# Kernel tuning notes

Measured on AMD Instinct MI355X. Metric: run time of the kernel, lower is better.

Reference implementation:

```python
import jax, jax.numpy as jnp
import numpy as np

NUM_NODES = 100000
NUM_EDGES = 100000
NNZ = 1600000
D_IN = 64
D_OUT = 64


def setup_inputs() -> dict:
    key = jax.random.key(0)
    k1, k2, k3, k4 = jax.random.split(key, 4)
    X = jax.random.normal(k1, (NUM_NODES, D_IN), dtype=jnp.float32)
    V = jax.random.randint(k2, (NNZ,), 0, NUM_NODES, dtype=jnp.int64)
    E = jax.random.randint(k3, (NNZ,), 0, NUM_EDGES, dtype=jnp.int64)
    S_features = jnp.zeros((1,), dtype=jnp.float32)  # unused by forward
    W = jax.random.normal(k4, (D_OUT, D_IN), dtype=jnp.float32) / np.sqrt(D_IN)
    b = jnp.zeros((D_OUT,), dtype=jnp.float32)
    return {"X": X, "V": V, "E": E, "S_features": S_features, "W": W, "b": b}


def reference(X, V, E, S_features, W, b):
    # linear projection (nn.Linear stores W as [out, in])
    Xp = X @ W.T + b                                   # [N, D_out]

    ones = jnp.ones((V.shape[0],), dtype=jnp.float32)
    cnt_e = jax.ops.segment_sum(ones, E, num_segments=NUM_EDGES)   # edge sizes
    D_v = jax.ops.segment_sum(ones, V, num_segments=NUM_NODES)     # node degrees

    # Y = scatter_mean(X[V], E): per-hyperedge mean of member node features
    Xve = Xp[V]                                        # [nnz, D_out]
    Y = jax.ops.segment_sum(Xve, E, num_segments=NUM_EDGES)
    Y = Y / jnp.maximum(cnt_e, 1.0)[:, None]

    # _De: torch scatter_reduce(reduce='mean', include_self=True) over zeros:
    # mean includes the initial self value 0 -> sum / (count + 1)
    De_sum = jax.ops.segment_sum(D_v[V], E, num_segments=NUM_EDGES)
    De = De_sum / (cnt_e + 1.0)
    De_inv = jnp.where(De > 0, jax.lax.rsqrt(jnp.maximum(De, 1e-30)), 1.0)
    Y = De_inv[:, None] * Y

    # scatter back to nodes
    Xev = Y[E]                                         # [nnz, D_out]
    Xn = jax.ops.segment_sum(Xev, V, num_segments=NUM_NODES)
    Dv_inv = jnp.where(D_v > 0, jax.lax.rsqrt(jnp.maximum(D_v, 1e-30)), 0.0)
    out = Dv_inv[:, None] * Xn                         # [N, D_out]
    # is_last=True: no relu / dropout
    return out
```

## Files before the change

### kernel.cpp

```cpp
#include <hip/hip_runtime.h>
#include <hip/hip_bf16.h>

#define NUM_NODES 100000
#define NUM_EDGES 100000
#define NNZ       1600000
#define D         64

#define BKT     128
#define NBKT_E  ((NUM_EDGES + BKT - 1) / BKT)
#define NBKT_V  ((NUM_NODES + BKT - 1) / BKT)
#define NBKT_TOT (NBKT_E + NBKT_V)
#define CAP     2816

#define TILE 8192
#define NT_SIDE ((NNZ + TILE - 1) / TILE)

#define GEMM_ROWS 32
#define NGEMM (NUM_NODES / GEMM_ROWS)

__device__ inline unsigned pack_bf16x2(float a, float b) {
  unsigned ua = __float_as_uint(a), ub = __float_as_uint(b);
  ua = (ua + 0x7fffu + ((ua >> 16) & 1u)) >> 16;
  ub = (ub + 0x7fffu + ((ub >> 16) & 1u)) >> 16;
  return ua | (ub << 16);
}
__device__ inline void unpack_acc(unsigned u, float& lo, float& hi) {
  lo = __uint_as_float(u << 16);
  hi = __uint_as_float(u & 0xffff0000u);
}
__device__ inline void acc_row(const uint4& w, float* acc) {
  float lo, hi;
  unpack_acc(w.x, lo, hi); acc[0] += lo; acc[1] += hi;
  unpack_acc(w.y, lo, hi); acc[2] += lo; acc[3] += hi;
  unpack_acc(w.z, lo, hi); acc[4] += lo; acc[5] += hi;
  unpack_acc(w.w, lo, hi); acc[6] += lo; acc[7] += hi;
}

__global__ __launch_bounds__(1024, 4) void bin_tile_k(
    const int* __restrict__ V, const int* __restrict__ E,
    int* __restrict__ curb, unsigned* __restrict__ pair) {
  __shared__ unsigned stage[TILE];
  __shared__ unsigned short stageb[TILE];
  __shared__ int hist[NBKT_E];
  __shared__ int gbase[NBKT_E];
  __shared__ int lcur[NBKT_E];
  __shared__ int wsum[16];

  const int t = threadIdx.x;
  const int side = (blockIdx.x >= NT_SIDE) ? 1 : 0;
  const int bt = blockIdx.x - side * NT_SIDE;
  const int j0 = bt * TILE;
  const int n = (NNZ - j0 < TILE) ? (NNZ - j0) : TILE;
  const int cbase = side ? NBKT_E : 0;

  for (int i = t; i < NBKT_E; i += 1024) hist[i] = 0;
  __syncthreads();

  int vj[8], ej[8];
#pragma unroll
  for (int k = 0; k < 8; ++k) {
    const int jj = t + k * 1024;
    int v = -1, e = 0;
    if (jj < n) {
      v = V[j0 + jj];
      e = E[j0 + jj];
    }
    vj[k] = v; ej[k] = e;
    if (v >= 0) atomicAdd(&hist[(side ? v : e) >> 7], 1);
  }
  __syncthreads();

  {
    const int lane = t & 63, wid = t >> 6;
    const int cb = (t < NBKT_E) ? hist[t] : 0;
    int s = cb;
#pragma unroll
    for (int d = 1; d < 64; d <<= 1) {
      const int y = __shfl_up(s, d, 64);
      if (lane >= d) s += y;
    }
    if (lane == 63) wsum[wid] = s;
    __syncthreads();
    if (wid == 0) {
      int ws = (lane < 16) ? wsum[lane] : 0;
#pragma unroll
      for (int d = 1; d < 16; d <<= 1) {
        const int y = __shfl_up(ws, d, 64);
        if (lane >= d) ws += y;
      }
      if (lane < 16) wsum[lane] = ws;
    }
    __syncthreads();
    const int incl = s + (wid > 0 ? wsum[wid - 1] : 0);
    if (t < NBKT_E) {
      const int excl = incl - cb;
      lcur[t] = excl;
      const int rb = cb ? atomicAdd(&curb[cbase + t], cb) : 0;
      gbase[t] = (cbase + t) * CAP + rb - excl;
    }
  }
  __syncthreads();

#pragma unroll
  for (int k = 0; k < 8; ++k) {
    const int v = vj[k];
    if (v >= 0) {
      const int e = ej[k];
      const int key = side ? v : e;
      const int src = side ? e : v;
      const int b = key >> 7;
      const unsigned w = ((unsigned)src << 7) | (unsigned)(key & 127);
      const int pos = atomicAdd(&lcur[b], 1);
      stage[pos] = w;
      stageb[pos] = (unsigned short)b;
    }
  }
  __syncthreads();

  for (int sI = t; sI < n; sI += 1024) {
    pair[gbase[stageb[sI]] + sI] = stage[sI];
  }
}

#define DG_SMEM 24832
__global__ __launch_bounds__(256) void deg_gemm_k(
    const int* __restrict__ curb, const unsigned* __restrict__ pair,
    int* __restrict__ cnt_v,
    const float* __restrict__ X, const float* __restrict__ W,
    const float* __restrict__ bvec, unsigned short* __restrict__ Xpb) {
  __shared__ __align__(16) char smem[DG_SMEM];
  const int t = threadIdx.x;

  if (blockIdx.x < NBKT_V) {
    int* rcnt = (int*)smem;
    const int b = blockIdx.x;
    const int base = (NBKT_E + b) * CAP;
    int n = curb[NBKT_E + b];
    if (n > CAP) n = CAP;
    if (t < BKT) rcnt[t] = 0;
    __syncthreads();
    for (int j = t; j < n; j += 256) {
      atomicAdd(&rcnt[pair[base + j] & 127u], 1);
    }
    __syncthreads();
    const int v = b * BKT + t;
    if (t < BKT && v < NUM_NODES) cnt_v[v] = rcnt[t];
  } else {
    float* Wl = (float*)smem;
    float* Xl = (float*)(smem + 16640);
    const int g = blockIdx.x - NBKT_V;

    for (int j = t; j < D * D; j += 256) Wl[(j >> 6) * 65 + (j & 63)] = W[j];
    const int row0 = g * GEMM_ROWS;
    const float4* X4 = (const float4*)(X + (size_t)row0 * D);
    float4* Xl4 = (float4*)Xl;
    for (int j = t; j < GEMM_ROWS * (D / 4); j += 256) Xl4[j] = X4[j];
    __syncthreads();

    const int c = t & 63;
    const int rq = t >> 6;
    float acc[8];
#pragma unroll
    for (int i = 0; i < 8; ++i) acc[i] = 0.f;
#pragma unroll
    for (int k = 0; k < D; ++k) {
      const float w = Wl[c * 65 + k];
#pragma unroll
      for (int i = 0; i < 8; ++i)
        acc[i] = fmaf(Xl[(rq + i * 4) * D + k], w, acc[i]);
    }
    const float bias = bvec[c];
#pragma unroll
    for (int i = 0; i < 8; ++i) {
      const int r = row0 + rq + i * 4;
      const float v = acc[i] + bias;
      unsigned u = __float_as_uint(v);
      u = (u + 0x7fffu + ((u >> 16) & 1u)) >> 16;
      Xpb[(size_t)r * D + c] = (unsigned short)u;
    }
  }
}

__global__ __launch_bounds__(512) void edge_fused_k(
    const int* __restrict__ curb, const unsigned* __restrict__ pair,
    const int* __restrict__ cnt_v, const uint4* __restrict__ Xpb,
    uint4* __restrict__ Yb) {
  __shared__ unsigned seg[CAP];
  __shared__ int sorted_[CAP];
  __shared__ int rcnt[BKT];
  __shared__ int sc[BKT];
  __shared__ int lcur[BKT];
  const int b = blockIdx.x, t = threadIdx.x;
  const int base = b * CAP;
  int n = curb[b];
  if (n > CAP) n = CAP;
  const int e0 = b * BKT;
  const int nrows = (NUM_EDGES - e0 < BKT) ? (NUM_EDGES - e0) : BKT;

  if (t < BKT) rcnt[t] = 0;
  __syncthreads();

  for (int j = t; j < n; j += 512) {
    const unsigned w = pair[base + j];
    seg[j] = w;
    atomicAdd(&rcnt[w & 127u], 1);
  }
  __syncthreads();

  if (t < 64) {
    const int a = rcnt[2 * t], bb = rcnt[2 * t + 1];
    int s = a + bb;
#pragma unroll
    for (int d = 1; d < 64; d <<= 1) {
      const int y = __shfl_up(s, d, 64);
      if (t >= d) s += y;
    }
    sc[2 * t + 1] = s;
    sc[2 * t] = s - bb;
    lcur[2 * t + 1] = s - bb;
    lcur[2 * t] = s - bb - a;
  }
  __syncthreads();

  for (int j = t; j < n; j += 512) {
    const unsigned w = seg[j];
    const int pos = atomicAdd(&lcur[w & 127u], 1);
    sorted_[pos] = (int)(w >> 7);
  }
  __syncthreads();

  const int q = t & 7;
#pragma unroll
  for (int rr = 0; rr < 2; ++rr) {
    const int row = (t >> 3) + rr * 64;
    const int ne = rcnt[row];
    const int mb = sc[row] - ne;
    const int me = sc[row];
    float acc[8];
#pragma unroll
    for (int i = 0; i < 8; ++i) acc[i] = 0.f;
    float dsum = 0.f;
    int m = mb;
    for (; m + 7 < me; m += 8) {
      int vv[8];
#pragma unroll
      for (int i = 0; i < 8; ++i) vv[i] = sorted_[m + i];
      uint4 w[8];
#pragma unroll
      for (int i = 0; i < 8; ++i) w[i] = Xpb[vv[i] * 8 + q];
      float dd[8];
#pragma unroll
      for (int i = 0; i < 8; ++i) dd[i] = (float)cnt_v[vv[i]];
      dsum += ((dd[0] + dd[1]) + (dd[2] + dd[3])) +
              ((dd[4] + dd[5]) + (dd[6] + dd[7]));
#pragma unroll
      for (int i = 0; i < 8; ++i) acc_row(w[i], acc);
    }
    for (; m + 3 < me; m += 4) {
      int vv[4];
#pragma unroll
      for (int i = 0; i < 4; ++i) vv[i] = sorted_[m + i];
      uint4 w[4];
#pragma unroll
      for (int i = 0; i < 4; ++i) w[i] = Xpb[vv[i] * 8 + q];
      float dd[4];
#pragma unroll
      for (int i = 0; i < 4; ++i) dd[i] = (float)cnt_v[vv[i]];
      dsum += (dd[0] + dd[1]) + (dd[2] + dd[3]);
#pragma unroll
      for (int i = 0; i < 4; ++i) acc_row(w[i], acc);
    }
    for (; m < me; ++m) {
      const int v = sorted_[m];
      const uint4 w = Xpb[v * 8 + q];
      dsum += (float)cnt_v[v];
      acc_row(w, acc);
    }
    const float ce = (float)ne;
    const float De = dsum / (ce + 1.f);
    const float inv = (De > 0.f) ? rsqrtf(fmaxf(De, 1e-30f)) : 1.f;
    const float s = inv / fmaxf(ce, 1.f);
    if (row < nrows) {
      uint4 o;
      o.x = pack_bf16x2(acc[0] * s, acc[1] * s);
      o.y = pack_bf16x2(acc[2] * s, acc[3] * s);
      o.z = pack_bf16x2(acc[4] * s, acc[5] * s);
      o.w = pack_bf16x2(acc[6] * s, acc[7] * s);
      Yb[(e0 + row) * 8 + q] = o;
    }
  }
}

__global__ __launch_bounds__(512) void node_fused_k(
    const int* __restrict__ curb, const unsigned* __restrict__ pair,
    const uint4* __restrict__ Yb, float* __restrict__ Out) {
  __shared__ unsigned seg[CAP];
  __shared__ int sorted_[CAP];
  __shared__ int rcnt[BKT];
  __shared__ int sc[BKT];
  __shared__ int lcur[BKT];
  const int b = blockIdx.x, t = threadIdx.x;
  const int base = (NBKT_E + b) * CAP;
  int n = curb[NBKT_E + b];
  if (n > CAP) n = CAP;
  const int v0r = b * BKT;
  const int nrows = (NUM_NODES - v0r < BKT) ? (NUM_NODES - v0r) : BKT;

  if (t < BKT) rcnt[t] = 0;
  __syncthreads();

  for (int j = t; j < n; j += 512) {
    const unsigned w = pair[base + j];
    seg[j] = w;
    atomicAdd(&rcnt[w & 127u], 1);
  }
  __syncthreads();

  if (t < 64) {
    const int a = rcnt[2 * t], bb = rcnt[2 * t + 1];
    int s = a + bb;
#pragma unroll
    for (int d = 1; d < 64; d <<= 1) {
      const int y = __shfl_up(s, d, 64);
      if (t >= d) s += y;
    }
    sc[2 * t + 1] = s;
    sc[2 * t] = s - bb;
    lcur[2 * t + 1] = s - bb;
    lcur[2 * t] = s - bb - a;
  }
  __syncthreads();

  for (int j = t; j < n; j += 512) {
    const unsigned w = seg[j];
    const int pos = atomicAdd(&lcur[w & 127u], 1);
    sorted_[pos] = (int)(w >> 7);
  }
  __syncthreads();

  const int q = t & 7;
#pragma unroll
  for (int rr = 0; rr < 2; ++rr) {
    const int row = (t >> 3) + rr * 64;
    const int dv = rcnt[row];
    const int mb = sc[row] - dv;
    const int me = sc[row];
    float acc[8];
#pragma unroll
    for (int i = 0; i < 8; ++i) acc[i] = 0.f;
    int m = mb;
    for (; m + 7 < me; m += 8) {
      int ee[8];
#pragma unroll
      for (int i = 0; i < 8; ++i) ee[i] = sorted_[m + i];
      uint4 w[8];
#pragma unroll
      for (int i = 0; i < 8; ++i) w[i] = Yb[ee[i] * 8 + q];
#pragma unroll
      for (int i = 0; i < 8; ++i) acc_row(w[i], acc);
    }
    for (; m + 3 < me; m += 4) {
      int ee[4];
#pragma unroll
      for (int i = 0; i < 4; ++i) ee[i] = sorted_[m + i];
      uint4 w[4];
#pragma unroll
      for (int i = 0; i < 4; ++i) w[i] = Yb[ee[i] * 8 + q];
#pragma unroll
      for (int i = 0; i < 4; ++i) acc_row(w[i], acc);
    }
    for (; m < me; ++m) {
      acc_row(Yb[sorted_[m] * 8 + q], acc);
    }
    const float d = (float)dv;
    const float s = (d > 0.f) ? rsqrtf(d) : 0.f;
    if (row < nrows) {
      float4* O4 = (float4*)(Out + (size_t)(v0r + row) * D + q * 8);
      O4[0] = make_float4(acc[0] * s, acc[1] * s, acc[2] * s, acc[3] * s);
      O4[1] = make_float4(acc[4] * s, acc[5] * s, acc[6] * s, acc[7] * s);
    }
  }
}

extern "C" void kernel_launch(void* const* d_in, const int* in_sizes, int n_in,
                              void* d_out, int out_size, void* d_ws, size_t ws_size,
                              hipStream_t stream) {
  const float* X = (const float*)d_in[0];
  const int*   V = (const int*)d_in[1];
  const int*   E = (const int*)d_in[2];
  const float* W = (const float*)d_in[4];
  const float* b = (const float*)d_in[5];
  float* Out = (float*)d_out;

  unsigned short* Xpb = (unsigned short*)d_ws;
  unsigned short* Ybu = Xpb + (size_t)NUM_NODES * D;
  int*      curb   = (int*)(Ybu + (size_t)NUM_EDGES * D);
  int*      cnt_v  = curb + NBKT_TOT;
  unsigned* pair   = (unsigned*)(cnt_v + NUM_NODES);

  hipMemsetAsync(curb, 0, NBKT_TOT * sizeof(int), stream);
  bin_tile_k<<<2 * NT_SIDE, 1024, 0, stream>>>(V, E, curb, pair);
  deg_gemm_k<<<NBKT_V + NGEMM, 256, 0, stream>>>(
      curb, pair, cnt_v, X, W, b, Xpb);
  edge_fused_k<<<NBKT_E, 512, 0, stream>>>(
      curb, pair, cnt_v, (const uint4*)Xpb, (uint4*)Ybu);
  node_fused_k<<<NBKT_V, 512, 0, stream>>>(
      curb, pair, (const uint4*)Ybu, Out);
}
```

Measured before the change: 194.7 us.

## Move per-bucket local sort into the GEMM stage and slim gather kernels

Moves the per-bucket counting sort of edge and node buckets out of the edge and node gather kernels into the combined stage/GEMM kernel. That kernel writes the sorted indices back into the pair buffer along with per-row offsets, so it overlaps with the projection GEMM blocks. The gather kernels now read indices directly from global memory instead of LDS and drop their large shared arrays, which may raise occupancy. The bin kernel also reloads V/E in the scatter pass instead of holding them in registers. In exchange there is an extra global write and read of the pair buffer, and the 8-wide unrolled gather loop is removed.

Measured after the change: 199.8 us. 1.03x slower.

```diff
diff --git a/kernel.cpp b/kernel.cpp
--- a/kernel.cpp
+++ b/kernel.cpp
@@ -56,17 +56,13 @@
   for (int i = t; i < NBKT_E; i += 1024) hist[i] = 0;
   __syncthreads();
 
-  int vj[8], ej[8];
-#pragma unroll
-  for (int k = 0; k < 8; ++k) {
-    const int jj = t + k * 1024;
-    int v = -1, e = 0;
-    if (jj < n) {
-      v = V[j0 + jj];
-      e = E[j0 + jj];
-    }
-    vj[k] = v; ej[k] = e;
-    if (v >= 0) atomicAdd(&hist[(side ? v : e) >> 7], 1);
+#pragma unroll
+  for (int k = 0; k < TILE / 1024; ++k) {
+    const int j = j0 + t + k * 1024;
+    if (j - j0 < n) {
+      const int key = side ? V[j] : E[j];
+      atomicAdd(&hist[key >> 7], 1);
+    }
   }
   __syncthreads();
 
@@ -102,10 +98,10 @@
   __syncthreads();
 
 #pragma unroll
-  for (int k = 0; k < 8; ++k) {
-    const int v = vj[k];
-    if (v >= 0) {
-      const int e = ej[k];
+  for (int k = 0; k < TILE / 1024; ++k) {
+    const int j = j0 + t + k * 1024;
+    if (j - j0 < n) {
+      const int v = V[j], e = E[j];
       const int key = side ? v : e;
       const int src = side ? e : v;
       const int b = key >> 7;
@@ -122,33 +118,70 @@
   }
 }
 
-#define DG_SMEM 24832
-__global__ __launch_bounds__(256) void deg_gemm_k(
-    const int* __restrict__ curb, const unsigned* __restrict__ pair,
-    int* __restrict__ cnt_v,
+#define SG_SMEM 24832
+__global__ __launch_bounds__(256) void stage_gemm_k(
+    const int* __restrict__ curb, unsigned* __restrict__ pair,
+    int* __restrict__ soff, int* __restrict__ cnt_v,
     const float* __restrict__ X, const float* __restrict__ W,
     const float* __restrict__ bvec, unsigned short* __restrict__ Xpb) {
-  __shared__ __align__(16) char smem[DG_SMEM];
+  __shared__ __align__(16) char smem[SG_SMEM];
   const int t = threadIdx.x;
 
-  if (blockIdx.x < NBKT_V) {
-    int* rcnt = (int*)smem;
+  if (blockIdx.x < NBKT_TOT) {
+    unsigned* seg = (unsigned*)smem;
+    int* sorted_ = (int*)(smem + 11264);
+    int* rcnt = (int*)(smem + 22528);
+    int* sc   = (int*)(smem + 23040);
+    int* lcur = (int*)(smem + 23552);
     const int b = blockIdx.x;
-    const int base = (NBKT_E + b) * CAP;
-    int n = curb[NBKT_E + b];
+    const int base = b * CAP;
+    int n = curb[b];
     if (n > CAP) n = CAP;
+
     if (t < BKT) rcnt[t] = 0;
     __syncthreads();
+
     for (int j = t; j < n; j += 256) {
-      atomicAdd(&rcnt[pair[base + j] & 127u], 1);
-    }
-    __syncthreads();
-    const int v = b * BKT + t;
-    if (t < BKT && v < NUM_NODES) cnt_v[v] = rcnt[t];
+      const unsigned w = pair[base + j];
+      seg[j] = w;
+      atomicAdd(&rcnt[w & 127u], 1);
+    }
+    __syncthreads();
+
+    if (t < 64) {
+      const int a = rcnt[2 * t], bb = rcnt[2 * t + 1];
+      int s = a + bb;
+#pragma unroll
+      for (int d = 1; d < 64; d <<= 1) {
+        const int y = __shfl_up(s, d, 64);
+        if (t >= d) s += y;
+      }
+      sc[2 * t + 1] = s;
+      sc[2 * t] = s - bb;
+      lcur[2 * t + 1] = s - bb;
+      lcur[2 * t] = s - bb - a;
+    }
+    __syncthreads();
+
+    for (int j = t; j < n; j += 256) {
+      const unsigned w = seg[j];
+      const int pos = atomicAdd(&lcur[w & 127u], 1);
+      sorted_[pos] = (int)(w >> 7);
+    }
+    __syncthreads();
+
+    for (int j = t; j < n; j += 256) pair[base + j] = (unsigned)sorted_[j];
+    if (t < BKT) {
+      soff[b * BKT + t] = sc[t];
+      if (b >= NBKT_E) {
+        const int v = (b - NBKT_E) * BKT + t;
+        if (v < NUM_NODES) cnt_v[v] = rcnt[t];
+      }
+    }
   } else {
     float* Wl = (float*)smem;
     float* Xl = (float*)(smem + 16640);
-    const int g = blockIdx.x - NBKT_V;
+    const int g = blockIdx.x - NBKT_TOT;
 
     for (int j = t; j < D * D; j += 256) Wl[(j >> 6) * 65 + (j & 63)] = W[j];
     const int row0 = g * GEMM_ROWS;
@@ -181,85 +214,35 @@
   }
 }
 
-__global__ __launch_bounds__(512) void edge_fused_k(
-    const int* __restrict__ curb, const unsigned* __restrict__ pair,
+__global__ __launch_bounds__(512) void edge_gather_k(
+    const unsigned* __restrict__ pair, const int* __restrict__ soff,
     const int* __restrict__ cnt_v, const uint4* __restrict__ Xpb,
     uint4* __restrict__ Yb) {
-  __shared__ unsigned seg[CAP];
-  __shared__ int sorted_[CAP];
-  __shared__ int rcnt[BKT];
   __shared__ int sc[BKT];
-  __shared__ int lcur[BKT];
   const int b = blockIdx.x, t = threadIdx.x;
   const int base = b * CAP;
-  int n = curb[b];
-  if (n > CAP) n = CAP;
   const int e0 = b * BKT;
   const int nrows = (NUM_EDGES - e0 < BKT) ? (NUM_EDGES - e0) : BKT;
 
-  if (t < BKT) rcnt[t] = 0;
-  __syncthreads();
-
-  for (int j = t; j < n; j += 512) {
-    const unsigned w = pair[base + j];
-    seg[j] = w;
-    atomicAdd(&rcnt[w & 127u], 1);
-  }
-  __syncthreads();
-
-  if (t < 64) {
-    const int a = rcnt[2 * t], bb = rcnt[2 * t + 1];
-    int s = a + bb;
-#pragma unroll
-    for (int d = 1; d < 64; d <<= 1) {
-      const int y = __shfl_up(s, d, 64);
-      if (t >= d) s += y;
-    }
-    sc[2 * t + 1] = s;
-    sc[2 * t] = s - bb;
-    lcur[2 * t + 1] = s - bb;
-    lcur[2 * t] = s - bb - a;
-  }
-  __syncthreads();
-
-  for (int j = t; j < n; j += 512) {
-    const unsigned w = seg[j];
-    const int pos = atomicAdd(&lcur[w & 127u], 1);
-    sorted_[pos] = (int)(w >> 7);
-  }
+  if (t < BKT) sc[t] = soff[b * BKT + t];
   __syncthreads();
 
   const int q = t & 7;
 #pragma unroll
   for (int rr = 0; rr < 2; ++rr) {
     const int row = (t >> 3) + rr * 64;
-    const int ne = rcnt[row];
-    const int mb = sc[row] - ne;
     const int me = sc[row];
+    const int mb = (row > 0) ? sc[row - 1] : 0;
+    const int ne = me - mb;
     float acc[8];
 #pragma unroll
     for (int i = 0; i < 8; ++i) acc[i] = 0.f;
     float dsum = 0.f;
     int m = mb;
-    for (; m + 7 < me; m += 8) {
-      int vv[8];
-#pragma unroll
-      for (int i = 0; i < 8; ++i) vv[i] = sorted_[m + i];
-      uint4 w[8];
-#pragma unroll
-      for (int i = 0; i < 8; ++i) w[i] = Xpb[vv[i] * 8 + q];
-      float dd[8];
-#pragma unroll
-      for (int i = 0; i < 8; ++i) dd[i] = (float)cnt_v[vv[i]];
-      dsum += ((dd[0] + dd[1]) + (dd[2] + dd[3])) +
-              ((dd[4] + dd[5]) + (dd[6] + dd[7]));
-#pragma unroll
-      for (int i = 0; i < 8; ++i) acc_row(w[i], acc);
-    }
     for (; m + 3 < me; m += 4) {
       int vv[4];
 #pragma unroll
-      for (int i = 0; i < 4; ++i) vv[i] = sorted_[m + i];
+      for (int i = 0; i < 4; ++i) vv[i] = (int)pair[base + m + i];
       uint4 w[4];
 #pragma unroll
       for (int i = 0; i < 4; ++i) w[i] = Xpb[vv[i] * 8 + q];
@@ -271,7 +254,7 @@
       for (int i = 0; i < 4; ++i) acc_row(w[i], acc);
     }
     for (; m < me; ++m) {
-      const int v = sorted_[m];
+      const int v = (int)pair[base + m];
       const uint4 w = Xpb[v * 8 + q];
       dsum += (float)cnt_v[v];
       acc_row(w, acc);
@@ -291,78 +274,33 @@
   }
 }
 
-__global__ __launch_bounds__(512) void node_fused_k(
-    const int* __restrict__ curb, const unsigned* __restrict__ pair,
+__global__ __launch_bounds__(512) void node_gather_k(
+    const unsigned* __restrict__ pair, const int* __restrict__ soff,
     const uint4* __restrict__ Yb, float* __restrict__ Out) {
-  __shared__ unsigned seg[CAP];
-  __shared__ int sorted_[CAP];
-  __shared__ int rcnt[BKT];
   __shared__ int sc[BKT];
-  __shared__ int lcur[BKT];
   const int b = blockIdx.x, t = threadIdx.x;
   const int base = (NBKT_E + b) * CAP;
-  int n = curb[NBKT_E + b];
-  if (n > CAP) n = CAP;
   const int v0r = b * BKT;
   const int nrows = (NUM_NODES - v0r < BKT) ? (NUM_NODES - v0r) : BKT;
 
-  if (t < BKT) rcnt[t] = 0;
-  __syncthreads();
-
-  for (int j = t; j < n; j += 512) {
-    const unsigned w = pair[base + j];
-    seg[j] = w;
-    atomicAdd(&rcnt[w & 127u], 1);
-  }
-  __syncthreads();
-
-  if (t < 64) {
-    const int a = rcnt[2 * t], bb = rcnt[2 * t + 1];
-    int s = a + bb;
-#pragma unroll
-    for (int d = 1; d < 64; d <<= 1) {
-      const int y = __shfl_up(s, d, 64);
-      if (t >= d) s += y;
-    }
-    sc[2 * t + 1] = s;
-    sc[2 * t] = s - bb;
-    lcur[2 * t + 1] = s - bb;
-    lcur[2 * t] = s - bb - a;
-  }
-  __syncthreads();
-
-  for (int j = t; j < n; j += 512) {
-    const unsigned w = seg[j];
-    const int pos = atomicAdd(&lcur[w & 127u], 1);
-    sorted_[pos] = (int)(w >> 7);
-  }
+  if (t < BKT) sc[t] = soff[(NBKT_E + b) * BKT + t];
   __syncthreads();
 
   const int q = t & 7;
 #pragma unroll
   for (int rr = 0; rr < 2; ++rr) {
     const int row = (t >> 3) + rr * 64;
-    const int dv = rcnt[row];
-    const int mb = sc[row] - dv;
     const int me = sc[row];
+    const int mb = (row > 0) ? sc[row - 1] : 0;
+    const int dv = me - mb;
     float acc[8];
 #pragma unroll
     for (int i = 0; i < 8; ++i) acc[i] = 0.f;
     int m = mb;
-    for (; m + 7 < me; m += 8) {
-      int ee[8];
-#pragma unroll
-      for (int i = 0; i < 8; ++i) ee[i] = sorted_[m + i];
-      uint4 w[8];
-#pragma unroll
-      for (int i = 0; i < 8; ++i) w[i] = Yb[ee[i] * 8 + q];
-#pragma unroll
-      for (int i = 0; i < 8; ++i) acc_row(w[i], acc);
-    }
     for (; m + 3 < me; m += 4) {
       int ee[4];
 #pragma unroll
-      for (int i = 0; i < 4; ++i) ee[i] = sorted_[m + i];
+      for (int i = 0; i < 4; ++i) ee[i] = (int)pair[base + m + i];
       uint4 w[4];
 #pragma unroll
       for (int i = 0; i < 4; ++i) w[i] = Yb[ee[i] * 8 + q];
@@ -370,7 +308,7 @@
       for (int i = 0; i < 4; ++i) acc_row(w[i], acc);
     }
     for (; m < me; ++m) {
-      acc_row(Yb[sorted_[m] * 8 + q], acc);
+      acc_row(Yb[(int)pair[base + m] * 8 + q], acc);
     }
     const float d = (float)dv;
     const float s = (d > 0.f) ? rsqrtf(d) : 0.f;
@@ -396,14 +334,15 @@
   unsigned short* Ybu = Xpb + (size_t)NUM_NODES * D;
   int*      curb   = (int*)(Ybu + (size_t)NUM_EDGES * D);
   int*      cnt_v  = curb + NBKT_TOT;
-  unsigned* pair   = (unsigned*)(cnt_v + NUM_NODES);
+  int*      soff   = cnt_v + NUM_NODES;
+  unsigned* pair   = (unsigned*)(soff + NBKT_TOT * BKT);
 
   hipMemsetAsync(curb, 0, NBKT_TOT * sizeof(int), stream);
   bin_tile_k<<<2 * NT_SIDE, 1024, 0, stream>>>(V, E, curb, pair);
-  deg_gemm_k<<<NBKT_V + NGEMM, 256, 0, stream>>>(
-      curb, pair, cnt_v, X, W, b, Xpb);
-  edge_fused_k<<<NBKT_E, 512, 0, stream>>>(
-      curb, pair, cnt_v, (const uint4*)Xpb, (uint4*)Ybu);
-  node_fused_k<<<NBKT_V, 512, 0, stream>>>(
-      curb, pair, (const uint4*)Ybu, Out);
-}
+  stage_gemm_k<<<NBKT_TOT + NGEMM, 256, 0, stream>>>(
+      curb, pair, soff, cnt_v, X, W, b, Xpb);
+  edge_gather_k<<<NBKT_E, 512, 0, stream>>>(
+      pair, soff, cnt_v, (const uint4*)Xpb, (uint4*)Ybu);
+  node_gather_k<<<NBKT_V, 512, 0, stream>>>(
+      pair, soff, (const uint4*)Ybu, Out);
+}
```
